# Kernel optimization log

Hardware: AMD Instinct MI355X
Metric: run time of the kernel (lower is better)

## Reference

```python
import jax, jax.numpy as jnp
import numpy as np

WIN = 9
EPS = 1e-05


def box_sum(x, win):
    # Separable box-filter sum, exactly equal to conv2d with an all-ones
    p = win // 2
    kh = jnp.ones((1, 1, win, 1), dtype=x.dtype)
    kw = jnp.ones((1, 1, 1, win), dtype=x.dtype)
    dn = jax.lax.conv_dimension_numbers(x.shape, kh.shape, ('NCHW', 'OIHW', 'NCHW'))
    x = jax.lax.conv_general_dilated(x, kh, (1, 1), [(p, p), (0, 0)], dimension_numbers=dn)
    x = jax.lax.conv_general_dilated(x, kw, (1, 1), [(0, 0), (p, p)], dimension_numbers=dn)
    return x


def setup_inputs() -> dict:
    key = jax.random.key(0)
    k1, k2 = jax.random.split(key)
    I = jax.random.normal(k1, (16, 1, 512, 512), dtype=jnp.float32)
    J = jax.random.normal(k2, (16, 1, 512, 512), dtype=jnp.float32)
    return {"I": I, "J": J}


def reference(I, J):
    win = WIN
    win_size = win * win
    I2 = I * I
    J2 = J * J
    IJ = I * J
    I_sum = box_sum(I, win)
    J_sum = box_sum(J, win)
    I2_sum = box_sum(I2, win)
    J2_sum = box_sum(J2, win)
    IJ_sum = box_sum(IJ, win)
    u_I = I_sum / win_size
    u_J = J_sum / win_size
    cross = IJ_sum - u_J * I_sum - u_I * J_sum + u_I * u_J * win_size
    I_var = I2_sum - 2 * u_I * I_sum + u_I * u_I * win_size
    J_var = J2_sum - 2 * u_J * J_sum + u_J * u_J * win_size
    cc = cross * cross / (I_var * J_var + EPS)
    return 1.0 - jnp.mean(cc)
```

## Files before the change

kernel.cpp:

```cpp
#include <hip/hip_runtime.h>

#define HH 512
#define WW 512
#define NIMG 16
#define EPSF 1e-5f
#define INV81 (1.0f / 81.0f)

__device__ __forceinline__ float dpp_shr1(float x) {
    return __int_as_float(__builtin_amdgcn_update_dpp(
        0, __float_as_int(x), 0x138, 0xF, 0xF, true));
}
__device__ __forceinline__ float dpp_shl1(float x) {
    return __int_as_float(__builtin_amdgcn_update_dpp(
        0, __float_as_int(x), 0x130, 0xF, 0xF, true));
}

__global__ __launch_bounds__(512, 4) void ncc_main(const float* __restrict__ Iin,
                                                   const float* __restrict__ Jin,
                                                   float* __restrict__ part) {
    __shared__ float4 ring4[16][2][128];
    __shared__ float wsum[8];

    const int tid  = threadIdx.x;
    const int lane = tid & 63;
    const int w    = tid >> 6;
    const int xcd  = blockIdx.x & 7;
    const int idx  = blockIdx.x >> 3;
    const int n    = (xcd << 1) | (idx >> 5);
    const int y0   = (idx & 31) << 4;
    const int c0   = lane << 3;

    const float* Ib = Iin + (size_t)n * (HH * WW);
    const float* Jb = Jin + (size_t)n * (HH * WW);

    auto gload = [&](int r, float4& a0, float4& a1, float4& b0, float4& b1) {
        if (r >= 0 && r < HH) {
            const float4* pI = (const float4*)(Ib + (size_t)r * WW + c0);
            const float4* pJ = (const float4*)(Jb + (size_t)r * WW + c0);
            a0 = pI[0]; a1 = pI[1]; b0 = pJ[0]; b1 = pJ[1];
        } else {
            a0 = a1 = b0 = b1 = make_float4(0.f, 0.f, 0.f, 0.f);
        }
    };
    auto swrite = [&](int r, const float4& a0, const float4& a1,
                             const float4& b0, const float4& b1) {
        const int sl = (r + 16) & 15;
        ring4[sl][0][lane]      = a0;
        ring4[sl][0][64 + lane] = a1;
        ring4[sl][1][lane]      = b0;
        ring4[sl][1][64 + lane] = b1;
    };

    {
        float4 p0, p1, q0, q1, r0, r1, s0, s1;
        gload(y0 - 4 + w, p0, p1, q0, q1);
        gload(y0 + 4 + w, r0, r1, s0, s1);
        swrite(y0 - 4 + w, p0, p1, q0, q1);
        swrite(y0 + 4 + w, r0, r1, s0, s1);
    }
    __syncthreads();

    float4 na0, na1, nb0, nb1;
    gload(y0 + 12 + w, na0, na1, nb0, nb1);

    auto hbox = [&](const float (&C)[8], float (&B)[8]) {
        float H[16];
        #pragma unroll
        for (int k = 0; k < 4; ++k) H[k] = dpp_shr1(C[4 + k]);
        #pragma unroll
        for (int k = 0; k < 8; ++k) H[4 + k] = C[k];
        #pragma unroll
        for (int k = 0; k < 4; ++k) H[12 + k] = dpp_shl1(C[k]);
        float s = ((H[0] + H[1]) + (H[2] + H[3])) + ((H[4] + H[5]) + (H[6] + H[7])) + H[8];
        B[0] = s;
        #pragma unroll
        for (int i = 1; i < 8; ++i) { s += H[i + 8] - H[i - 1]; B[i] = s; }
    };

    float local = 0.f;

    auto dorow = [&](int R) {
        float SI[8], SJ[8], SI2[8], SJ2[8], SIJ[8];
        #pragma unroll
        for (int c = 0; c < 8; ++c) { SI[c]=0.f; SJ[c]=0.f; SI2[c]=0.f; SJ2[c]=0.f; SIJ[c]=0.f; }
        #pragma unroll
        for (int k = 0; k < 9; ++k) {
            const int sl = (R - 4 + k + 16) & 15;
            const float4 i0 = ring4[sl][0][lane];
            const float4 i1 = ring4[sl][0][64 + lane];
            const float4 j0 = ring4[sl][1][lane];
            const float4 j1 = ring4[sl][1][64 + lane];
            const float ai[8] = {i0.x, i0.y, i0.z, i0.w, i1.x, i1.y, i1.z, i1.w};
            const float bj[8] = {j0.x, j0.y, j0.z, j0.w, j1.x, j1.y, j1.z, j1.w};
            #pragma unroll
            for (int c = 0; c < 8; ++c) {
                SI[c] += ai[c];  SJ[c] += bj[c];
                SI2[c] = fmaf(ai[c], ai[c], SI2[c]);
                SJ2[c] = fmaf(bj[c], bj[c], SJ2[c]);
                SIJ[c] = fmaf(ai[c], bj[c], SIJ[c]);
            }
        }
        float BI[8], BJ[8], BI2[8], BJ2[8], BIJ[8];
        hbox(SI, BI); hbox(SJ, BJ); hbox(SI2, BI2); hbox(SJ2, BJ2); hbox(SIJ, BIJ);
        #pragma unroll
        for (int c = 0; c < 8; ++c) {
            const float tI = BI[c] * INV81;
            const float tJ = BJ[c] * INV81;
            const float cross = fmaf(-tI, BJ[c], BIJ[c]);
            const float Iv    = fmaf(-tI, BI[c], BI2[c]);
            const float Jv    = fmaf(-tJ, BJ[c], BJ2[c]);
            const float den   = fmaf(Iv, Jv, EPSF);
            local = fmaf(cross * cross, __builtin_amdgcn_rcpf(den), local);
        }
    };

    dorow(y0 + w);
    __syncthreads();
    swrite(y0 + 12 + w, na0, na1, nb0, nb1);
    __syncthreads();
    dorow(y0 + 8 + w);

    #pragma unroll
    for (int off = 32; off > 0; off >>= 1) local += __shfl_down(local, off);
    if (lane == 0) wsum[w] = local;
    __syncthreads();
    if (tid == 0) {
        float b = 0.f;
        #pragma unroll
        for (int k = 0; k < 8; ++k) b += wsum[k];
        part[blockIdx.x] = b;
    }
}

__global__ __launch_bounds__(512) void ncc_final(const float* __restrict__ part,
                                                 float* __restrict__ out) {
    __shared__ float s[8];
    const int tid  = threadIdx.x;
    const int lane = tid & 63;
    const int w    = tid >> 6;
    float v = part[tid];
    #pragma unroll
    for (int off = 32; off > 0; off >>= 1) v += __shfl_down(v, off);
    if (lane == 0) s[w] = v;
    __syncthreads();
    if (tid == 0) {
        float t = 0.f;
        #pragma unroll
        for (int k = 0; k < 8; ++k) t += s[k];
        out[0] = 1.0f - t * (1.0f / (float)((size_t)NIMG * HH * WW));
    }
}

extern "C" void kernel_launch(void* const* d_in, const int* in_sizes, int n_in,
                              void* d_out, int out_size, void* d_ws, size_t ws_size,
                              hipStream_t stream) {
    const float* I = (const float*)d_in[0];
    const float* J = (const float*)d_in[1];
    float* out  = (float*)d_out;
    float* part = (float*)d_ws;

    ncc_main<<<512, 512, 0, stream>>>(I, J, part);
    ncc_final<<<1, 512, 0, stream>>>(part, out);
}
```

Measured before the change: 15.93 us.

## Process 32-row tiles per block with sliding vertical sums over row pairs

Each block now covers 32 rows instead of 16 and halves the grid to 256 blocks. The shared ring grows to 24 slots, so the 8-row halo is loaded for 32 output rows rather than 16. Each wave computes two adjacent rows, deriving the second vertical sum from the first by adding one row and subtracting one, which saves most of the second 9-row accumulation. The cost is fewer blocks (one per CU on a 256-CU part), lower occupancy hints, and more LDS per block, which may reduce latency hiding.

Measured after the change: 19.53 us. 22.6% more time.

```diff
diff --git a/kernel.cpp b/kernel.cpp
--- a/kernel.cpp
+++ b/kernel.cpp
@@ -15,10 +15,10 @@
         0, __float_as_int(x), 0x130, 0xF, 0xF, true));
 }
 
-__global__ __launch_bounds__(512, 4) void ncc_main(const float* __restrict__ Iin,
+__global__ __launch_bounds__(512, 2) void ncc_main(const float* __restrict__ Iin,
                                                    const float* __restrict__ Jin,
                                                    float* __restrict__ part) {
-    __shared__ float4 ring4[16][2][128];
+    __shared__ float4 ring4[24][2][128];
     __shared__ float wsum[8];
 
     const int tid  = threadIdx.x;
@@ -26,14 +26,15 @@
     const int w    = tid >> 6;
     const int xcd  = blockIdx.x & 7;
     const int idx  = blockIdx.x >> 3;
-    const int n    = (xcd << 1) | (idx >> 5);
-    const int y0   = (idx & 31) << 4;
+    const int n    = (xcd << 1) | (idx >> 4);
+    const int y0   = (idx & 15) << 5;
     const int c0   = lane << 3;
 
     const float* Ib = Iin + (size_t)n * (HH * WW);
     const float* Jb = Jin + (size_t)n * (HH * WW);
 
-    auto gload = [&](int r, float4& a0, float4& a1, float4& b0, float4& b1) {
+    auto gload = [&](int rr, float4& a0, float4& a1, float4& b0, float4& b1) {
+        const int r = y0 - 4 + rr;
         if (r >= 0 && r < HH) {
             const float4* pI = (const float4*)(Ib + (size_t)r * WW + c0);
             const float4* pJ = (const float4*)(Jb + (size_t)r * WW + c0);
@@ -42,26 +43,39 @@
             a0 = a1 = b0 = b1 = make_float4(0.f, 0.f, 0.f, 0.f);
         }
     };
-    auto swrite = [&](int r, const float4& a0, const float4& a1,
-                             const float4& b0, const float4& b1) {
-        const int sl = (r + 16) & 15;
+    auto swrite = [&](int rr, const float4& a0, const float4& a1,
+                              const float4& b0, const float4& b1) {
+        const int sl = rr < 24 ? rr : rr - 24;
         ring4[sl][0][lane]      = a0;
         ring4[sl][0][64 + lane] = a1;
         ring4[sl][1][lane]      = b0;
         ring4[sl][1][64 + lane] = b1;
     };
+    auto readslot = [&](int rr, float (&ai)[8], float (&bj)[8]) {
+        const int sl = rr < 24 ? rr : rr - 24;
+        const float4 i0 = ring4[sl][0][lane];
+        const float4 i1 = ring4[sl][0][64 + lane];
+        const float4 j0 = ring4[sl][1][lane];
+        const float4 j1 = ring4[sl][1][64 + lane];
+        ai[0]=i0.x; ai[1]=i0.y; ai[2]=i0.z; ai[3]=i0.w;
+        ai[4]=i1.x; ai[5]=i1.y; ai[6]=i1.z; ai[7]=i1.w;
+        bj[0]=j0.x; bj[1]=j0.y; bj[2]=j0.z; bj[3]=j0.w;
+        bj[4]=j1.x; bj[5]=j1.y; bj[6]=j1.z; bj[7]=j1.w;
+    };
 
     {
-        float4 p0, p1, q0, q1, r0, r1, s0, s1;
-        gload(y0 - 4 + w, p0, p1, q0, q1);
-        gload(y0 + 4 + w, r0, r1, s0, s1);
-        swrite(y0 - 4 + w, p0, p1, q0, q1);
-        swrite(y0 + 4 + w, r0, r1, s0, s1);
+        float4 p0, p1, q0, q1;
+        #pragma unroll
+        for (int k = 0; k < 3; ++k) {
+            gload(3 * w + k, p0, p1, q0, q1);
+            swrite(3 * w + k, p0, p1, q0, q1);
+        }
     }
     __syncthreads();
 
-    float4 na0, na1, nb0, nb1;
-    gload(y0 + 12 + w, na0, na1, nb0, nb1);
+    float4 na0, na1, nb0, nb1, ma0, ma1, mb0, mb1;
+    gload(24 + 2 * w, na0, na1, nb0, nb1);
+    gload(25 + 2 * w, ma0, ma1, mb0, mb1);
 
     auto hbox = [&](const float (&C)[8], float (&B)[8]) {
         float H[16];
@@ -79,27 +93,9 @@
 
     float local = 0.f;
 
-    auto dorow = [&](int R) {
-        float SI[8], SJ[8], SI2[8], SJ2[8], SIJ[8];
-        #pragma unroll
-        for (int c = 0; c < 8; ++c) { SI[c]=0.f; SJ[c]=0.f; SI2[c]=0.f; SJ2[c]=0.f; SIJ[c]=0.f; }
-        #pragma unroll
-        for (int k = 0; k < 9; ++k) {
-            const int sl = (R - 4 + k + 16) & 15;
-            const float4 i0 = ring4[sl][0][lane];
-            const float4 i1 = ring4[sl][0][64 + lane];
-            const float4 j0 = ring4[sl][1][lane];
-            const float4 j1 = ring4[sl][1][64 + lane];
-            const float ai[8] = {i0.x, i0.y, i0.z, i0.w, i1.x, i1.y, i1.z, i1.w};
-            const float bj[8] = {j0.x, j0.y, j0.z, j0.w, j1.x, j1.y, j1.z, j1.w};
-            #pragma unroll
-            for (int c = 0; c < 8; ++c) {
-                SI[c] += ai[c];  SJ[c] += bj[c];
-                SI2[c] = fmaf(ai[c], ai[c], SI2[c]);
-                SJ2[c] = fmaf(bj[c], bj[c], SJ2[c]);
-                SIJ[c] = fmaf(ai[c], bj[c], SIJ[c]);
-            }
-        }
+    auto ccrow = [&](const float (&SI)[8], const float (&SJ)[8],
+                     const float (&SI2)[8], const float (&SJ2)[8],
+                     const float (&SIJ)[8]) {
         float BI[8], BJ[8], BI2[8], BJ2[8], BIJ[8];
         hbox(SI, BI); hbox(SJ, BJ); hbox(SI2, BI2); hbox(SJ2, BJ2); hbox(SIJ, BIJ);
         #pragma unroll
@@ -114,11 +110,49 @@
         }
     };
 
-    dorow(y0 + w);
+    auto dopair = [&](int rrA) {
+        float SI[8], SJ[8], SI2[8], SJ2[8], SIJ[8];
+        #pragma unroll
+        for (int c = 0; c < 8; ++c) { SI[c]=0.f; SJ[c]=0.f; SI2[c]=0.f; SJ2[c]=0.f; SIJ[c]=0.f; }
+        float ai[8], bj[8];
+        #pragma unroll
+        for (int k = 0; k < 9; ++k) {
+            readslot(rrA + k, ai, bj);
+            #pragma unroll
+            for (int c = 0; c < 8; ++c) {
+                SI[c] += ai[c];  SJ[c] += bj[c];
+                SI2[c] = fmaf(ai[c], ai[c], SI2[c]);
+                SJ2[c] = fmaf(bj[c], bj[c], SJ2[c]);
+                SIJ[c] = fmaf(ai[c], bj[c], SIJ[c]);
+            }
+        }
+        ccrow(SI, SJ, SI2, SJ2, SIJ);
+
+        readslot(rrA + 9, ai, bj);
+        #pragma unroll
+        for (int c = 0; c < 8; ++c) {
+            SI[c] += ai[c];  SJ[c] += bj[c];
+            SI2[c] = fmaf(ai[c], ai[c], SI2[c]);
+            SJ2[c] = fmaf(bj[c], bj[c], SJ2[c]);
+            SIJ[c] = fmaf(ai[c], bj[c], SIJ[c]);
+        }
+        readslot(rrA, ai, bj);
+        #pragma unroll
+        for (int c = 0; c < 8; ++c) {
+            SI[c] -= ai[c];  SJ[c] -= bj[c];
+            SI2[c] = fmaf(-ai[c], ai[c], SI2[c]);
+            SJ2[c] = fmaf(-bj[c], bj[c], SJ2[c]);
+            SIJ[c] = fmaf(-ai[c], bj[c], SIJ[c]);
+        }
+        ccrow(SI, SJ, SI2, SJ2, SIJ);
+    };
+
+    dopair(2 * w);
     __syncthreads();
-    swrite(y0 + 12 + w, na0, na1, nb0, nb1);
+    swrite(24 + 2 * w, na0, na1, nb0, nb1);
+    swrite(25 + 2 * w, ma0, ma1, mb0, mb1);
     __syncthreads();
-    dorow(y0 + 8 + w);
+    dopair(16 + 2 * w);
 
     #pragma unroll
     for (int off = 32; off > 0; off >>= 1) local += __shfl_down(local, off);
@@ -132,9 +166,9 @@
     }
 }
 
-__global__ __launch_bounds__(512) void ncc_final(const float* __restrict__ part,
+__global__ __launch_bounds__(256) void ncc_final(const float* __restrict__ part,
                                                  float* __restrict__ out) {
-    __shared__ float s[8];
+    __shared__ float s[4];
     const int tid  = threadIdx.x;
     const int lane = tid & 63;
     const int w    = tid >> 6;
@@ -144,9 +178,7 @@
     if (lane == 0) s[w] = v;
     __syncthreads();
     if (tid == 0) {
-        float t = 0.f;
-        #pragma unroll
-        for (int k = 0; k < 8; ++k) t += s[k];
+        float t = (s[0] + s[1]) + (s[2] + s[3]);
         out[0] = 1.0f - t * (1.0f / (float)((size_t)NIMG * HH * WW));
     }
 }
@@ -159,6 +191,6 @@
     float* out  = (float*)d_out;
     float* part = (float*)d_ws;
 
-    ncc_main<<<512, 512, 0, stream>>>(I, J, part);
-    ncc_final<<<1, 512, 0, stream>>>(part, out);
+    ncc_main<<<256, 512, 0, stream>>>(I, J, part);
+    ncc_final<<<1, 256, 0, stream>>>(part, out);
 }
```

## Halve rows per block and double grid, dropping the in-block ring pipeline

Applied to the files above, without the earlier changes.

Each block now computes 8 output rows instead of 16, and the grid grows from 512 to 1024 blocks. The prefetch and second ring-buffer stage go away: each block loads its 16 rows, including halo, in one pass and does a single compute phase. The aim is more parallelism and fewer barriers per block. The cost is a larger halo overhead, since 16 rows are loaded for 8 outputs instead of 24 for 16, and a final reduction that grows to 1024 partials.

New measurement: 16.01 us (median of 2 runs). No clear change (+0.5%).

```diff
diff --git a/kernel.cpp b/kernel.cpp
--- a/kernel.cpp
+++ b/kernel.cpp
@@ -26,14 +26,15 @@
     const int w    = tid >> 6;
     const int xcd  = blockIdx.x & 7;
     const int idx  = blockIdx.x >> 3;
-    const int n    = (xcd << 1) | (idx >> 5);
-    const int y0   = (idx & 31) << 4;
+    const int n    = (xcd << 1) | (idx >> 6);
+    const int y0   = (idx & 63) << 3;
     const int c0   = lane << 3;
 
     const float* Ib = Iin + (size_t)n * (HH * WW);
     const float* Jb = Jin + (size_t)n * (HH * WW);
 
-    auto gload = [&](int r, float4& a0, float4& a1, float4& b0, float4& b1) {
+    auto gload = [&](int rr, float4& a0, float4& a1, float4& b0, float4& b1) {
+        const int r = y0 - 4 + rr;
         if (r >= 0 && r < HH) {
             const float4* pI = (const float4*)(Ib + (size_t)r * WW + c0);
             const float4* pJ = (const float4*)(Jb + (size_t)r * WW + c0);
@@ -42,26 +43,22 @@
             a0 = a1 = b0 = b1 = make_float4(0.f, 0.f, 0.f, 0.f);
         }
     };
-    auto swrite = [&](int r, const float4& a0, const float4& a1,
-                             const float4& b0, const float4& b1) {
-        const int sl = (r + 16) & 15;
-        ring4[sl][0][lane]      = a0;
-        ring4[sl][0][64 + lane] = a1;
-        ring4[sl][1][lane]      = b0;
-        ring4[sl][1][64 + lane] = b1;
+    auto swrite = [&](int rr, const float4& a0, const float4& a1,
+                              const float4& b0, const float4& b1) {
+        ring4[rr][0][lane]      = a0;
+        ring4[rr][0][64 + lane] = a1;
+        ring4[rr][1][lane]      = b0;
+        ring4[rr][1][64 + lane] = b1;
     };
 
     {
         float4 p0, p1, q0, q1, r0, r1, s0, s1;
-        gload(y0 - 4 + w, p0, p1, q0, q1);
-        gload(y0 + 4 + w, r0, r1, s0, s1);
-        swrite(y0 - 4 + w, p0, p1, q0, q1);
-        swrite(y0 + 4 + w, r0, r1, s0, s1);
+        gload(2 * w,     p0, p1, q0, q1);
+        gload(2 * w + 1, r0, r1, s0, s1);
+        swrite(2 * w,     p0, p1, q0, q1);
+        swrite(2 * w + 1, r0, r1, s0, s1);
     }
     __syncthreads();
-
-    float4 na0, na1, nb0, nb1;
-    gload(y0 + 12 + w, na0, na1, nb0, nb1);
 
     auto hbox = [&](const float (&C)[8], float (&B)[8]) {
         float H[16];
@@ -79,13 +76,13 @@
 
     float local = 0.f;
 
-    auto dorow = [&](int R) {
+    {
         float SI[8], SJ[8], SI2[8], SJ2[8], SIJ[8];
         #pragma unroll
         for (int c = 0; c < 8; ++c) { SI[c]=0.f; SJ[c]=0.f; SI2[c]=0.f; SJ2[c]=0.f; SIJ[c]=0.f; }
         #pragma unroll
         for (int k = 0; k < 9; ++k) {
-            const int sl = (R - 4 + k + 16) & 15;
+            const int sl = w + k;
             const float4 i0 = ring4[sl][0][lane];
             const float4 i1 = ring4[sl][0][64 + lane];
             const float4 j0 = ring4[sl][1][lane];
@@ -112,13 +109,7 @@
             const float den   = fmaf(Iv, Jv, EPSF);
             local = fmaf(cross * cross, __builtin_amdgcn_rcpf(den), local);
         }
-    };
-
-    dorow(y0 + w);
-    __syncthreads();
-    swrite(y0 + 12 + w, na0, na1, nb0, nb1);
-    __syncthreads();
-    dorow(y0 + 8 + w);
+    }
 
     #pragma unroll
     for (int off = 32; off > 0; off >>= 1) local += __shfl_down(local, off);
@@ -132,9 +123,9 @@
     }
 }
 
-__global__ __launch_bounds__(512) void ncc_final(const float* __restrict__ part,
-                                                 float* __restrict__ out) {
-    __shared__ float s[8];
+__global__ __launch_bounds__(1024) void ncc_final(const float* __restrict__ part,
+                                                  float* __restrict__ out) {
+    __shared__ float s[16];
     const int tid  = threadIdx.x;
     const int lane = tid & 63;
     const int w    = tid >> 6;
@@ -146,7 +137,7 @@
     if (tid == 0) {
         float t = 0.f;
         #pragma unroll
-        for (int k = 0; k < 8; ++k) t += s[k];
+        for (int k = 0; k < 16; ++k) t += s[k];
         out[0] = 1.0f - t * (1.0f / (float)((size_t)NIMG * HH * WW));
     }
 }
@@ -159,6 +150,6 @@
     float* out  = (float*)d_out;
     float* part = (float*)d_ws;
 
-    ncc_main<<<512, 512, 0, stream>>>(I, J, part);
-    ncc_final<<<1, 512, 0, stream>>>(part, out);
+    ncc_main<<<1024, 512, 0, stream>>>(I, J, part);
+    ncc_final<<<1, 1024, 0, stream>>>(part, out);
 }
```
